# Kernel tuning notes

Measured on AMD Instinct MI355X. Metric: run time of the kernel, lower is better.

The kernel has to match this reference:

```python
import jax, jax.numpy as jnp
import numpy as np

HEADS = 8
DIM_HEAD = 64
SCALE = 10.0
EPS = 1e-12  # F.normalize eps


def setup_inputs() -> dict:
    key = jax.random.key(0)
    k1, k2, k3, k4 = jax.random.split(key, 4)
    dim, hidden = 256, HEADS * DIM_HEAD
    x = jax.random.normal(k1, (8, dim, 32, 32), dtype=jnp.float32)
    w_qkv = jax.random.normal(k2, (3 * hidden, dim), dtype=jnp.float32) * (1.0 / np.sqrt(dim))
    w_out = jax.random.normal(k3, (dim, hidden), dtype=jnp.float32) * (1.0 / np.sqrt(hidden))
    b_out = jax.random.normal(k4, (dim,), dtype=jnp.float32) * 0.01
    return {"x": x, "w_qkv": w_qkv, "w_out": w_out, "b_out": b_out}


def _l2norm_last(t):
    # matches F.normalize(t, dim=-1): t / max(||t||_2, eps)
    n = jnp.sqrt(jnp.sum(t * t, axis=-1, keepdims=True))
    return t / jnp.maximum(n, EPS)


def reference(x, w_qkv, w_out, b_out):
    b, c, hh, ww = x.shape
    n = hh * ww
    # 1x1 conv == channel matmul
    qkv = jnp.einsum('bcxy,oc->boxy', x, w_qkv)  # (b, 3*hidden, h, w)
    q, k, v = jnp.split(qkv, 3, axis=1)
    # 'b (h c) x y -> b h c (x y)'
    to_heads = lambda t: t.reshape(b, HEADS, DIM_HEAD, n)
    q, k, v = to_heads(q), to_heads(k), to_heads(v)
    # NOTE: l2norm over the LAST axis = spatial token axis n (faithful to source)
    q = _l2norm_last(q)
    k = _l2norm_last(k)
    sim = jnp.einsum('bhdi,bhdj->bhij', q, k) * SCALE  # (b, h, n, n)
    attn = jax.nn.softmax(sim, axis=-1)
    out = jnp.einsum('bhij,bhdj->bhid', attn, v)  # (b, h, n, d)
    # 'b h (x y) d -> b (h d) x y'
    out = out.transpose(0, 1, 3, 2).reshape(b, HEADS * DIM_HEAD, hh, ww)
    return jnp.einsum('bcxy,oc->boxy', out, w_out) + b_out[None, :, None, None]
```

## Files before the change

kernel.cpp:

```cpp
#include <hip/hip_runtime.h>
#include <math.h>

#define NHEADS 8
#define DHEAD  64
#define HIDDEN 512
#define CIN    256
#define NTOK   1024
#define QK_SCALE 10.0f
#define LOG2E 1.44269504088896f

typedef __bf16 bf16x8 __attribute__((ext_vector_type(8)));
typedef float  f32x4  __attribute__((ext_vector_type(4)));
typedef unsigned short u16x8 __attribute__((ext_vector_type(8)));

__device__ inline unsigned short f2bf(float f) {
    unsigned u = __builtin_bit_cast(unsigned, f);
    u = (u + 0x7FFFu + ((u >> 16) & 1u)) >> 16;
    return (unsigned short)u;
}

__device__ inline bf16x8 cvt8(const float* p) {
    float4 a = *(const float4*)p;
    float4 b = *(const float4*)(p + 4);
    u16x8 t;
    t[0] = f2bf(a.x); t[1] = f2bf(a.y); t[2] = f2bf(a.z); t[3] = f2bf(a.w);
    t[4] = f2bf(b.x); t[5] = f2bf(b.y); t[6] = f2bf(b.z); t[7] = f2bf(b.w);
    return __builtin_bit_cast(bf16x8, t);
}

__global__ __launch_bounds__(256)
void cvt_x_kernel(const float* __restrict__ x, unsigned short* __restrict__ xt) {
    const int b  = blockIdx.z;
    const int c0 = blockIdx.y * 64;
    const int n0 = blockIdx.x * 64;
    const float* src = x + ((size_t)b * CIN + c0) * NTOK + n0;
    unsigned short* dst = xt + ((size_t)b * NTOK + n0) * CIN + c0;

    __shared__ float T[64][65];
    const int t = threadIdx.x;
    {
        const int nq = t & 15, cg = t >> 4;
        #pragma unroll
        for (int rr = 0; rr < 4; ++rr) {
            const int c = cg + rr * 16;
            float4 v = *(const float4*)(src + (size_t)c * NTOK + nq * 4);
            T[c][nq * 4 + 0] = v.x;
            T[c][nq * 4 + 1] = v.y;
            T[c][nq * 4 + 2] = v.z;
            T[c][nq * 4 + 3] = v.w;
        }
    }
    __syncthreads();
    {
        const int n = t >> 2, cq = t & 3;
        alignas(16) unsigned short tmp[16];
        #pragma unroll
        for (int e = 0; e < 16; ++e)
            tmp[e] = f2bf(T[cq * 16 + e][n]);
        *(uint4*)(dst + (size_t)n * CIN + cq * 16)     = *(uint4*)&tmp[0];
        *(uint4*)(dst + (size_t)n * CIN + cq * 16 + 8) = *(uint4*)&tmp[8];
    }
}

__global__ __launch_bounds__(256)
void cvt_w_kernel(const float* __restrict__ wq, const float* __restrict__ wo,
                  unsigned short* __restrict__ wqb, unsigned short* __restrict__ wob) {
    const size_t i = ((size_t)blockIdx.x * 256 + threadIdx.x) * 8;
    if (i < (size_t)1536 * 256) {
        *(bf16x8*)(wqb + i) = cvt8(wq + i);
    } else {
        const size_t j = i - (size_t)1536 * 256;
        *(bf16x8*)(wob + j) = cvt8(wo + j);
    }
}

__global__ __launch_bounds__(256)
void gemm1_kernel(const unsigned short* __restrict__ wqb,
                  const unsigned short* __restrict__ xt,
                  float* __restrict__ qt,
                  unsigned short* __restrict__ vb,
                  float* __restrict__ ss) {
    const int b  = blockIdx.z;
    const int bm = blockIdx.y * 128;
    const int bn = blockIdx.x * 128;
    const int wave = threadIdx.x >> 6, lane = threadIdx.x & 63;
    const int lo = lane & 15, hi = lane >> 4;
    const int wm = bm + (wave >> 1) * 64;
    const int wn = bn + (wave & 1) * 64;

    const unsigned short* Ab = wqb + (size_t)(wm + lo) * CIN + hi * 8;
    const unsigned short* Bb = xt + ((size_t)b * NTOK + wn + lo) * CIN + hi * 8;

    f32x4 acc[4][4];
    #pragma unroll
    for (int mi = 0; mi < 4; ++mi)
        #pragma unroll
        for (int ni = 0; ni < 4; ++ni) acc[mi][ni] = (f32x4){0.f, 0.f, 0.f, 0.f};

    for (int k0 = 0; k0 < CIN; k0 += 32) {
        bf16x8 a[4], bf[4];
        #pragma unroll
        for (int mi = 0; mi < 4; ++mi) a[mi]  = *(const bf16x8*)(Ab + (size_t)mi * 16 * CIN + k0);
        #pragma unroll
        for (int ni = 0; ni < 4; ++ni) bf[ni] = *(const bf16x8*)(Bb + (size_t)ni * 16 * CIN + k0);
        #pragma unroll
        for (int mi = 0; mi < 4; ++mi)
            #pragma unroll
            for (int ni = 0; ni < 4; ++ni)
                acc[mi][ni] = __builtin_amdgcn_mfma_f32_16x16x32_bf16(a[mi], bf[ni], acc[mi][ni], 0, 0, 0);
    }

    __shared__ unsigned short VL[4][32][72];

    if (bm < 1024) {
        const int isK = (wm >= 512) ? 1 : 0;
        const int ch0 = wm & 511;
        const int head = ch0 >> 6;
        float* dst = qt + (((size_t)isK * 64 + b * 8 + head) * NTOK) * DHEAD;
        #pragma unroll
        for (int mi = 0; mi < 4; ++mi) {
            const int d = mi * 16 + hi * 4;
            #pragma unroll
            for (int ni = 0; ni < 4; ++ni) {
                const int n = wn + ni * 16 + lo;
                *(f32x4*)(dst + (size_t)n * DHEAD + d) = acc[mi][ni];
            }
        }
        float p[4][4];
        #pragma unroll
        for (int mi = 0; mi < 4; ++mi)
            #pragma unroll
            for (int r = 0; r < 4; ++r) {
                float s = 0.f;
                #pragma unroll
                for (int ni = 0; ni < 4; ++ni) s += acc[mi][ni][r] * acc[mi][ni][r];
                p[mi][r] = s;
            }
        #pragma unroll
        for (int off = 1; off < 16; off <<= 1)
            #pragma unroll
            for (int mi = 0; mi < 4; ++mi)
                #pragma unroll
                for (int r = 0; r < 4; ++r)
                    p[mi][r] += __shfl_xor(p[mi][r], off, 64);
        if (lo == 0) {
            #pragma unroll
            for (int mi = 0; mi < 4; ++mi)
                #pragma unroll
                for (int r = 0; r < 4; ++r)
                    atomicAdd(&ss[(size_t)b * 1024 + isK * 512 + ch0 + mi * 16 + hi * 4 + r], p[mi][r]);
        }
    } else {
        const int ch0 = wm - 1024;
        #pragma unroll
        for (int half = 0; half < 2; ++half) {
            #pragma unroll
            for (int mm = 0; mm < 2; ++mm) {
                const int mi = half * 2 + mm;
                #pragma unroll
                for (int ni = 0; ni < 4; ++ni)
                    #pragma unroll
                    for (int r = 0; r < 4; ++r)
                        VL[wave][mm * 16 + hi * 4 + r][ni * 16 + lo] = f2bf(acc[mi][ni][r]);
            }
            #pragma unroll
            for (int i = 0; i < 4; ++i) {
                const int flat = i * 64 + lane;
                const int row = flat >> 3, c = flat & 7;
                uint4 v = *(uint4*)&VL[wave][row][c * 8];
                const int ch = ch0 + half * 32 + row;
                *(uint4*)(vb + ((size_t)b * HIDDEN + ch) * NTOK + wn + c * 8) = v;
            }
        }
    }
}

__global__ __launch_bounds__(256)
void invn_kernel(const float* __restrict__ ss, float* __restrict__ invn) {
    const int i = blockIdx.x * 256 + threadIdx.x;
    invn[i] = 1.0f / fmaxf(sqrtf(ss[i]), 1e-12f);
}

__global__ __launch_bounds__(256)
void scale_cvt_kernel(const float* __restrict__ qt, const float* __restrict__ invn,
                      unsigned short* __restrict__ qs, unsigned short* __restrict__ ks) {
    const size_t idx = ((size_t)blockIdx.x * 256 + threadIdx.x) * 8;
    const size_t half = (size_t)64 * NTOK * DHEAD;
    const int isK = idx >= half;
    const size_t rem = idx - (size_t)isK * half;
    const int bh = (int)(rem >> 16);
    const int d0 = (int)(rem & 63);
    const int b  = bh >> 3;
    const int ch = isK * 512 + (bh & 7) * 64 + d0;
    const float scl = isK ? 1.0f : QK_SCALE;

    const float* ip = qt + idx;
    float4 v0 = *(const float4*)ip;
    float4 v1 = *(const float4*)(ip + 4);
    float4 s0 = *(const float4*)(invn + (size_t)b * 1024 + ch);
    float4 s1 = *(const float4*)(invn + (size_t)b * 1024 + ch + 4);
    u16x8 t;
    t[0] = f2bf(v0.x * s0.x * scl); t[1] = f2bf(v0.y * s0.y * scl);
    t[2] = f2bf(v0.z * s0.z * scl); t[3] = f2bf(v0.w * s0.w * scl);
    t[4] = f2bf(v1.x * s1.x * scl); t[5] = f2bf(v1.y * s1.y * scl);
    t[6] = f2bf(v1.z * s1.z * scl); t[7] = f2bf(v1.w * s1.w * scl);
    *(u16x8*)((isK ? ks : qs) + rem) = t;
}

__global__ __launch_bounds__(256)
void attn_mfma_kernel(const unsigned short* __restrict__ qs,
                      const unsigned short* __restrict__ ks,
                      const unsigned short* __restrict__ vb,
                      unsigned short* __restrict__ attn_t) {
    const int hw = blockIdx.x;
    const int virt = (hw & 7) * 64 + (hw >> 3);
    const int bh = virt >> 3;
    const int it = virt & 7;
    const int b = bh >> 3, h = bh & 7;

    const int lane = threadIdx.x & 63;
    const int wave = threadIdx.x >> 6;
    const int lo = lane & 15;
    const int hi = lane >> 4;
    const int iw = it * 128 + wave * 32;

    const unsigned short* qbh = qs + (size_t)bh * NTOK * DHEAD;
    const unsigned short* kbh = ks + (size_t)bh * NTOK * DHEAD;
    const unsigned short* vbh = vb + ((size_t)b * HIDDEN + h * DHEAD) * NTOK;

    __shared__ unsigned short Plds[4][4096];
    __shared__ float Tlds[4][16][69];
    char* pbase = (char*)&Plds[wave][0];

    bf16x8 aQ[2][2];
    #pragma unroll
    for (int f = 0; f < 2; ++f) {
        const unsigned short* qp = qbh + (size_t)(iw + f * 16 + lo) * DHEAD + hi * 8;
        aQ[f][0] = *(const bf16x8*)qp;
        aQ[f][1] = *(const bf16x8*)(qp + 32);
    }

    float m_r[2][4], l_r[2][4];
    #pragma unroll
    for (int f = 0; f < 2; ++f)
        #pragma unroll
        for (int r = 0; r < 4; ++r) { m_r[f][r] = -INFINITY; l_r[f][r] = 0.0f; }
    f32x4 acc[2][4];
    #pragma unroll
    for (int f = 0; f < 2; ++f)
        #pragma unroll
        for (int ds = 0; ds < 4; ++ds) acc[f][ds] = (f32x4){0.f, 0.f, 0.f, 0.f};

    for (int jt = 0; jt < 8; ++jt) {
        const int j0 = jt * 128;

        f32x4 s[2][8];
        #pragma unroll
        for (int js = 0; js < 8; ++js) {
            const unsigned short* kp = kbh + (size_t)(j0 + js * 16 + lo) * DHEAD + hi * 8;
            const bf16x8 bK0 = *(const bf16x8*)kp;
            const bf16x8 bK1 = *(const bf16x8*)(kp + 32);
            __builtin_amdgcn_s_setprio(1);
            #pragma unroll
            for (int f = 0; f < 2; ++f) {
                f32x4 c = (f32x4){0.f, 0.f, 0.f, 0.f};
                c = __builtin_amdgcn_mfma_f32_16x16x32_bf16(aQ[f][0], bK0, c, 0, 0, 0);
                c = __builtin_amdgcn_mfma_f32_16x16x32_bf16(aQ[f][1], bK1, c, 0, 0, 0);
                s[f][js] = c;
            }
            __builtin_amdgcn_s_setprio(0);
        }

        bf16x8 bV[4][4];
        #pragma unroll
        for (int ds = 0; ds < 4; ++ds)
            #pragma unroll
            for (int jj = 0; jj < 4; ++jj)
                bV[ds][jj] = *(const bf16x8*)(vbh + (size_t)(ds * 16 + lo) * NTOK + j0 + jj * 32 + hi * 8);

        #pragma unroll
        for (int f = 0; f < 2; ++f) {
            float mt[4];
            #pragma unroll
            for (int r = 0; r < 4; ++r)
                mt[r] = fmaxf(fmaxf(fmaxf(s[f][0][r], s[f][1][r]), fmaxf(s[f][2][r], s[f][3][r])),
                              fmaxf(fmaxf(s[f][4][r], s[f][5][r]), fmaxf(s[f][6][r], s[f][7][r])));
            #pragma unroll
            for (int off = 1; off < 16; off <<= 1)
                #pragma unroll
                for (int r = 0; r < 4; ++r)
                    mt[r] = fmaxf(mt[r], __shfl_xor(mt[r], off, 64));

            float corr[4];
            #pragma unroll
            for (int r = 0; r < 4; ++r) {
                const float mn = fmaxf(m_r[f][r], mt[r]);
                corr[r] = __builtin_amdgcn_exp2f((m_r[f][r] - mn) * LOG2E);
                m_r[f][r] = mn;
            }
            float rs[4] = {0.f, 0.f, 0.f, 0.f};
            #pragma unroll
            for (int js = 0; js < 8; ++js)
                #pragma unroll
                for (int r = 0; r < 4; ++r) {
                    const float pp = __builtin_amdgcn_exp2f((s[f][js][r] - m_r[f][r]) * LOG2E);
                    s[f][js][r] = pp;
                    rs[r] += pp;
                }
            #pragma unroll
            for (int off = 1; off < 16; off <<= 1)
                #pragma unroll
                for (int r = 0; r < 4; ++r)
                    rs[r] += __shfl_xor(rs[r], off, 64);
            #pragma unroll
            for (int r = 0; r < 4; ++r) l_r[f][r] = l_r[f][r] * corr[r] + rs[r];
            #pragma unroll
            for (int ds = 0; ds < 4; ++ds)
                #pragma unroll
                for (int r = 0; r < 4; ++r)
                    acc[f][ds][r] *= corr[r];

            #pragma unroll
            for (int js = 0; js < 8; ++js)
                #pragma unroll
                for (int r = 0; r < 4; ++r) {
                    const int row = f * 16 + hi * 4 + r;
                    const int byte = (row * 256 + (js * 16 + lo) * 2) ^ ((row & 7) << 4);
                    *(unsigned short*)(pbase + byte) = f2bf(s[f][js][r]);
                }
        }

        bf16x8 aP[2][4];
        #pragma unroll
        for (int f = 0; f < 2; ++f) {
            const int row = f * 16 + lo;
            const int swz = (lo & 7) << 4;
            #pragma unroll
            for (int jj = 0; jj < 4; ++jj)
                aP[f][jj] = *(const bf16x8*)(pbase + ((row * 256 + jj * 64 + hi * 16) ^ swz));
        }
        __builtin_amdgcn_s_setprio(1);
        #pragma unroll
        for (int ds = 0; ds < 4; ++ds)
            #pragma unroll
            for (int f = 0; f < 2; ++f)
                #pragma unroll
                for (int jj = 0; jj < 4; ++jj)
                    acc[f][ds] = __builtin_amdgcn_mfma_f32_16x16x32_bf16(aP[f][jj], bV[ds][jj], acc[f][ds], 0, 0, 0);
        __builtin_amdgcn_s_setprio(0);
    }

    #pragma unroll
    for (int f = 0; f < 2; ++f) {
        float invl[4];
        #pragma unroll
        for (int r = 0; r < 4; ++r) invl[r] = 1.0f / l_r[f][r];
        #pragma unroll
        for (int ds = 0; ds < 4; ++ds)
            #pragma unroll
            for (int r = 0; r < 4; ++r)
                Tlds[wave][hi * 4 + r][ds * 16 + lo] = acc[f][ds][r] * invl[r];
        {
            const int i = lane >> 2, ck = lane & 3;
            alignas(16) unsigned short tmp[16];
            #pragma unroll
            for (int e = 0; e < 16; ++e)
                tmp[e] = f2bf(Tlds[wave][i][ck * 16 + e]);
            unsigned short* dst = attn_t + ((size_t)b * NTOK + iw + f * 16 + i) * HIDDEN + h * DHEAD + ck * 16;
            *(uint4*)dst       = *(uint4*)&tmp[0];
            *(uint4*)(dst + 8) = *(uint4*)&tmp[8];
        }
    }
}

__global__ __launch_bounds__(128)
void gemm2_kernel(const unsigned short* __restrict__ wob,
                  const unsigned short* __restrict__ attn_t,
                  const float* __restrict__ b_out,
                  float* __restrict__ out) {
    const int b  = blockIdx.z;
    const int bm = blockIdx.y * 64;
    const int bn = blockIdx.x * 128;
    const int wave = threadIdx.x >> 6, lane = threadIdx.x & 63;
    const int lo = lane & 15, hi = lane >> 4;
    const int wn = bn + wave * 64;

    const unsigned short* Ab = wob + (size_t)(bm + lo) * HIDDEN + hi * 8;
    const unsigned short* Bb = attn_t + ((size_t)b * NTOK + wn + lo) * HIDDEN + hi * 8;

    f32x4 acc[4][4];
    #pragma unroll
    for (int mi = 0; mi < 4; ++mi)
        #pragma unroll
        for (int ni = 0; ni < 4; ++ni) acc[mi][ni] = (f32x4){0.f, 0.f, 0.f, 0.f};

    for (int k0 = 0; k0 < HIDDEN; k0 += 32) {
        bf16x8 a[4], bf[4];
        #pragma unroll
        for (int mi = 0; mi < 4; ++mi) a[mi]  = *(const bf16x8*)(Ab + (size_t)mi * 16 * HIDDEN + k0);
        #pragma unroll
        for (int ni = 0; ni < 4; ++ni) bf[ni] = *(const bf16x8*)(Bb + (size_t)ni * 16 * HIDDEN + k0);
        #pragma unroll
        for (int mi = 0; mi < 4; ++mi)
            #pragma unroll
            for (int ni = 0; ni < 4; ++ni)
                acc[mi][ni] = __builtin_amdgcn_mfma_f32_16x16x32_bf16(a[mi], bf[ni], acc[mi][ni], 0, 0, 0);
    }

    __shared__ float OL[2][32][69];
    #pragma unroll
    for (int half = 0; half < 2; ++half) {
        #pragma unroll
        for (int mm = 0; mm < 2; ++mm) {
            const int mi = half * 2 + mm;
            #pragma unroll
            for (int ni = 0; ni < 4; ++ni)
                #pragma unroll
                for (int r = 0; r < 4; ++r)
                    OL[wave][mm * 16 + hi * 4 + r][ni * 16 + lo] = acc[mi][ni][r];
        }
        #pragma unroll
        for (int i = 0; i < 8; ++i) {
            const int flat = i * 64 + lane;
            const int row = flat >> 4, c = flat & 15;
            float4 v = *(float4*)&OL[wave][row][c * 4];
            const int m = bm + half * 32 + row;
            const float bb = b_out[m];
            v.x += bb; v.y += bb; v.z += bb; v.w += bb;
            *(float4*)(out + ((size_t)b * CIN + m) * NTOK + wn + c * 4) = v;
        }
    }
}

extern "C" void kernel_launch(void* const* d_in, const int* in_sizes, int n_in,
                              void* d_out, int out_size, void* d_ws, size_t ws_size,
                              hipStream_t stream) {
    const float* x     = (const float*)d_in[0];
    const float* w_qkv = (const float*)d_in[1];
    const float* w_out = (const float*)d_in[2];
    const float* b_out = (const float*)d_in[3];
    float* out = (float*)d_out;

    char* ws = (char*)d_ws;
    unsigned short* xt  = (unsigned short*)(ws);
    unsigned short* wqb = (unsigned short*)(ws + 4194304);
    unsigned short* wob = (unsigned short*)(ws + 4980736);
    float*          ss  = (float*)(ws + 5242880);
    float*          inv = (float*)(ws + 5275648);
    unsigned short* qs  = (unsigned short*)(ws + 5308416);
    unsigned short* ks  = (unsigned short*)(ws + 13697024);
    unsigned short* vb  = (unsigned short*)(ws + 22085632);
    float*          qt  = (float*)(ws + 30474240);
    unsigned short* attn_t = (unsigned short*)(ws + 30474240);

    hipMemsetAsync(ss, 0, 8 * 1024 * sizeof(float), stream);

    cvt_x_kernel<<<dim3(16, 4, 8), 256, 0, stream>>>(x, xt);
    cvt_w_kernel<<<256, 256, 0, stream>>>(w_qkv, w_out, wqb, wob);

    gemm1_kernel<<<dim3(8, 12, 8), 256, 0, stream>>>(wqb, xt, qt, vb, ss);

    invn_kernel<<<32, 256, 0, stream>>>(ss, inv);
    scale_cvt_kernel<<<4096, 256, 0, stream>>>(qt, inv, qs, ks);

    attn_mfma_kernel<<<512, 256, 0, stream>>>(qs, ks, vb, attn_t);

    gemm2_kernel<<<dim3(8, 4, 8), 128, 0, stream>>>(wob, attn_t, b_out, out);
}
```

Baseline: 218.8 us.

## Split attention over key halves and merge partials in a combine kernel

The attention kernel now splits the key dimension into two halves (split-K flash decoding), doubling the grid from 512 to 1024 blocks and shrinking per-iteration tiles to 64 keys. Each half writes unnormalized fp32 partial outputs plus its row max and sum, and a new combine kernel merges them into bf16 attn_t. The separate invn kernel is folded into scale_cvt, saving a launch. The aim is better occupancy and more blocks across CUs, at the cost of extra fp32 partial traffic and an extra kernel launch.

Measured after the change: 227.4 us. 3.9% more time.

```diff
diff --git a/kernel.cpp b/kernel.cpp
--- a/kernel.cpp
+++ b/kernel.cpp
@@ -12,6 +12,7 @@
 typedef __bf16 bf16x8 __attribute__((ext_vector_type(8)));
 typedef float  f32x4  __attribute__((ext_vector_type(4)));
 typedef unsigned short u16x8 __attribute__((ext_vector_type(8)));
+typedef unsigned short u16x4 __attribute__((ext_vector_type(4)));
 
 __device__ inline unsigned short f2bf(float f) {
     unsigned u = __builtin_bit_cast(unsigned, f);
@@ -176,13 +177,7 @@
 }
 
 __global__ __launch_bounds__(256)
-void invn_kernel(const float* __restrict__ ss, float* __restrict__ invn) {
-    const int i = blockIdx.x * 256 + threadIdx.x;
-    invn[i] = 1.0f / fmaxf(sqrtf(ss[i]), 1e-12f);
-}
-
-__global__ __launch_bounds__(256)
-void scale_cvt_kernel(const float* __restrict__ qt, const float* __restrict__ invn,
+void scale_cvt_kernel(const float* __restrict__ qt, const float* __restrict__ ss,
                       unsigned short* __restrict__ qs, unsigned short* __restrict__ ks) {
     const size_t idx = ((size_t)blockIdx.x * 256 + threadIdx.x) * 8;
     const size_t half = (size_t)64 * NTOK * DHEAD;
@@ -197,8 +192,13 @@
     const float* ip = qt + idx;
     float4 v0 = *(const float4*)ip;
     float4 v1 = *(const float4*)(ip + 4);
-    float4 s0 = *(const float4*)(invn + (size_t)b * 1024 + ch);
-    float4 s1 = *(const float4*)(invn + (size_t)b * 1024 + ch + 4);
+    float4 q0 = *(const float4*)(ss + (size_t)b * 1024 + ch);
+    float4 q1 = *(const float4*)(ss + (size_t)b * 1024 + ch + 4);
+    float4 s0, s1;
+    s0.x = 1.0f / fmaxf(sqrtf(q0.x), 1e-12f); s0.y = 1.0f / fmaxf(sqrtf(q0.y), 1e-12f);
+    s0.z = 1.0f / fmaxf(sqrtf(q0.z), 1e-12f); s0.w = 1.0f / fmaxf(sqrtf(q0.w), 1e-12f);
+    s1.x = 1.0f / fmaxf(sqrtf(q1.x), 1e-12f); s1.y = 1.0f / fmaxf(sqrtf(q1.y), 1e-12f);
+    s1.z = 1.0f / fmaxf(sqrtf(q1.z), 1e-12f); s1.w = 1.0f / fmaxf(sqrtf(q1.w), 1e-12f);
     u16x8 t;
     t[0] = f2bf(v0.x * s0.x * scl); t[1] = f2bf(v0.y * s0.y * scl);
     t[2] = f2bf(v0.z * s0.z * scl); t[3] = f2bf(v0.w * s0.w * scl);
@@ -211,11 +211,13 @@
 void attn_mfma_kernel(const unsigned short* __restrict__ qs,
                       const unsigned short* __restrict__ ks,
                       const unsigned short* __restrict__ vb,
-                      unsigned short* __restrict__ attn_t) {
+                      float* __restrict__ po, float* __restrict__ pml) {
     const int hw = blockIdx.x;
-    const int virt = (hw & 7) * 64 + (hw >> 3);
-    const int bh = virt >> 3;
-    const int it = virt & 7;
+    const int virt = (hw & 7) * 128 + (hw >> 3);
+    const int bh = virt >> 4;
+    const int sub = virt & 15;
+    const int it = sub & 7;
+    const int js = sub >> 3;
     const int b = bh >> 3, h = bh & 7;
 
     const int lane = threadIdx.x & 63;
@@ -228,8 +230,8 @@
     const unsigned short* kbh = ks + (size_t)bh * NTOK * DHEAD;
     const unsigned short* vbh = vb + ((size_t)b * HIDDEN + h * DHEAD) * NTOK;
 
-    __shared__ unsigned short Plds[4][4096];
-    __shared__ float Tlds[4][16][69];
+    __shared__ unsigned short Plds[4][2048];
+    __shared__ float Tlds[4][16][68];
     char* pbase = (char*)&Plds[wave][0];
 
     bf16x8 aQ[2][2];
@@ -252,12 +254,20 @@
         for (int ds = 0; ds < 4; ++ds) acc[f][ds] = (f32x4){0.f, 0.f, 0.f, 0.f};
 
     for (int jt = 0; jt < 8; ++jt) {
-        const int j0 = jt * 128;
-
-        f32x4 s[2][8];
-        #pragma unroll
-        for (int js = 0; js < 8; ++js) {
-            const unsigned short* kp = kbh + (size_t)(j0 + js * 16 + lo) * DHEAD + hi * 8;
+        const int j0 = js * 512 + jt * 64;
+
+        bf16x8 bV[4][2];
+        #pragma unroll
+        for (int ds = 0; ds < 4; ++ds) {
+            const unsigned short* vp = vbh + (size_t)(ds * 16 + lo) * NTOK + j0 + hi * 8;
+            bV[ds][0] = *(const bf16x8*)vp;
+            bV[ds][1] = *(const bf16x8*)(vp + 32);
+        }
+
+        f32x4 s[2][4];
+        #pragma unroll
+        for (int jj = 0; jj < 4; ++jj) {
+            const unsigned short* kp = kbh + (size_t)(j0 + jj * 16 + lo) * DHEAD + hi * 8;
             const bf16x8 bK0 = *(const bf16x8*)kp;
             const bf16x8 bK1 = *(const bf16x8*)(kp + 32);
             __builtin_amdgcn_s_setprio(1);
@@ -266,25 +276,17 @@
                 f32x4 c = (f32x4){0.f, 0.f, 0.f, 0.f};
                 c = __builtin_amdgcn_mfma_f32_16x16x32_bf16(aQ[f][0], bK0, c, 0, 0, 0);
                 c = __builtin_amdgcn_mfma_f32_16x16x32_bf16(aQ[f][1], bK1, c, 0, 0, 0);
-                s[f][js] = c;
+                s[f][jj] = c;
             }
             __builtin_amdgcn_s_setprio(0);
         }
-
-        bf16x8 bV[4][4];
-        #pragma unroll
-        for (int ds = 0; ds < 4; ++ds)
-            #pragma unroll
-            for (int jj = 0; jj < 4; ++jj)
-                bV[ds][jj] = *(const bf16x8*)(vbh + (size_t)(ds * 16 + lo) * NTOK + j0 + jj * 32 + hi * 8);
 
         #pragma unroll
         for (int f = 0; f < 2; ++f) {
             float mt[4];
             #pragma unroll
             for (int r = 0; r < 4; ++r)
-                mt[r] = fmaxf(fmaxf(fmaxf(s[f][0][r], s[f][1][r]), fmaxf(s[f][2][r], s[f][3][r])),
-                              fmaxf(fmaxf(s[f][4][r], s[f][5][r]), fmaxf(s[f][6][r], s[f][7][r])));
+                mt[r] = fmaxf(fmaxf(s[f][0][r], s[f][1][r]), fmaxf(s[f][2][r], s[f][3][r]));
             #pragma unroll
             for (int off = 1; off < 16; off <<= 1)
                 #pragma unroll
@@ -300,11 +302,11 @@
             }
             float rs[4] = {0.f, 0.f, 0.f, 0.f};
             #pragma unroll
-            for (int js = 0; js < 8; ++js)
+            for (int jj = 0; jj < 4; ++jj)
                 #pragma unroll
                 for (int r = 0; r < 4; ++r) {
-                    const float pp = __builtin_amdgcn_exp2f((s[f][js][r] - m_r[f][r]) * LOG2E);
-                    s[f][js][r] = pp;
+                    const float pp = __builtin_amdgcn_exp2f((s[f][jj][r] - m_r[f][r]) * LOG2E);
+                    s[f][jj][r] = pp;
                     rs[r] += pp;
                 }
             #pragma unroll
@@ -321,56 +323,86 @@
                     acc[f][ds][r] *= corr[r];
 
             #pragma unroll
-            for (int js = 0; js < 8; ++js)
+            for (int jj = 0; jj < 4; ++jj)
                 #pragma unroll
                 for (int r = 0; r < 4; ++r) {
                     const int row = f * 16 + hi * 4 + r;
-                    const int byte = (row * 256 + (js * 16 + lo) * 2) ^ ((row & 7) << 4);
-                    *(unsigned short*)(pbase + byte) = f2bf(s[f][js][r]);
+                    const int byte = (row * 128 + (jj * 16 + lo) * 2) ^ ((row & 7) << 4);
+                    *(unsigned short*)(pbase + byte) = f2bf(s[f][jj][r]);
                 }
         }
 
-        bf16x8 aP[2][4];
+        bf16x8 aP[2][2];
         #pragma unroll
         for (int f = 0; f < 2; ++f) {
             const int row = f * 16 + lo;
             const int swz = (lo & 7) << 4;
-            #pragma unroll
-            for (int jj = 0; jj < 4; ++jj)
-                aP[f][jj] = *(const bf16x8*)(pbase + ((row * 256 + jj * 64 + hi * 16) ^ swz));
+            aP[f][0] = *(const bf16x8*)(pbase + ((row * 128 + hi * 16) ^ swz));
+            aP[f][1] = *(const bf16x8*)(pbase + ((row * 128 + 64 + hi * 16) ^ swz));
         }
         __builtin_amdgcn_s_setprio(1);
         #pragma unroll
         for (int ds = 0; ds < 4; ++ds)
             #pragma unroll
-            for (int f = 0; f < 2; ++f)
-                #pragma unroll
-                for (int jj = 0; jj < 4; ++jj)
-                    acc[f][ds] = __builtin_amdgcn_mfma_f32_16x16x32_bf16(aP[f][jj], bV[ds][jj], acc[f][ds], 0, 0, 0);
+            for (int f = 0; f < 2; ++f) {
+                acc[f][ds] = __builtin_amdgcn_mfma_f32_16x16x32_bf16(aP[f][0], bV[ds][0], acc[f][ds], 0, 0, 0);
+                acc[f][ds] = __builtin_amdgcn_mfma_f32_16x16x32_bf16(aP[f][1], bV[ds][1], acc[f][ds], 0, 0, 0);
+            }
         __builtin_amdgcn_s_setprio(0);
     }
 
+    float* pob = po + ((size_t)(js * 64 + bh) * NTOK + iw) * DHEAD;
     #pragma unroll
     for (int f = 0; f < 2; ++f) {
-        float invl[4];
-        #pragma unroll
-        for (int r = 0; r < 4; ++r) invl[r] = 1.0f / l_r[f][r];
         #pragma unroll
         for (int ds = 0; ds < 4; ++ds)
             #pragma unroll
             for (int r = 0; r < 4; ++r)
-                Tlds[wave][hi * 4 + r][ds * 16 + lo] = acc[f][ds][r] * invl[r];
-        {
-            const int i = lane >> 2, ck = lane & 3;
-            alignas(16) unsigned short tmp[16];
-            #pragma unroll
-            for (int e = 0; e < 16; ++e)
-                tmp[e] = f2bf(Tlds[wave][i][ck * 16 + e]);
-            unsigned short* dst = attn_t + ((size_t)b * NTOK + iw + f * 16 + i) * HIDDEN + h * DHEAD + ck * 16;
-            *(uint4*)dst       = *(uint4*)&tmp[0];
-            *(uint4*)(dst + 8) = *(uint4*)&tmp[8];
-        }
-    }
+                Tlds[wave][hi * 4 + r][ds * 16 + lo] = acc[f][ds][r];
+        #pragma unroll
+        for (int pass = 0; pass < 4; ++pass) {
+            const int flat = pass * 64 + lane;
+            const int row = flat >> 4, dq = flat & 15;
+            float4 v = *(float4*)&Tlds[wave][row][dq * 4];
+            *(float4*)(pob + (size_t)(f * 16 + row) * DHEAD + dq * 4) = v;
+        }
+        if (lo == 0) {
+            #pragma unroll
+            for (int r = 0; r < 4; ++r) {
+                const int row = iw + f * 16 + hi * 4 + r;
+                float2 ml = make_float2(m_r[f][r], l_r[f][r]);
+                *(float2*)(pml + ((size_t)(js * 64 + bh) * NTOK + row) * 2) = ml;
+            }
+        }
+    }
+}
+
+__global__ __launch_bounds__(256)
+void combine_kernel(const float* __restrict__ po, const float* __restrict__ pml,
+                    unsigned short* __restrict__ attn_t) {
+    const size_t fl = ((size_t)blockIdx.x * 256 + threadIdx.x) * 4;
+    const int bh  = (int)(fl >> 16);
+    const int rem = (int)(fl & 65535);
+    const int row = rem >> 6;
+    const int d   = rem & 63;
+    const int b = bh >> 3, h = bh & 7;
+    const size_t SS = (size_t)64 * NTOK * DHEAD;
+
+    const float2 ml1 = *(const float2*)(pml + ((size_t)bh * NTOK + row) * 2);
+    const float2 ml2 = *(const float2*)(pml + ((size_t)(64 + bh) * NTOK + row) * 2);
+    const float M  = fmaxf(ml1.x, ml2.x);
+    const float w1 = __builtin_amdgcn_exp2f((ml1.x - M) * LOG2E);
+    const float w2 = __builtin_amdgcn_exp2f((ml2.x - M) * LOG2E);
+    const float inv = 1.0f / (ml1.y * w1 + ml2.y * w2);
+
+    const float4 o1 = *(const float4*)(po + fl);
+    const float4 o2 = *(const float4*)(po + SS + fl);
+    u16x4 r;
+    r[0] = f2bf((o1.x * w1 + o2.x * w2) * inv);
+    r[1] = f2bf((o1.y * w1 + o2.y * w2) * inv);
+    r[2] = f2bf((o1.z * w1 + o2.z * w2) * inv);
+    r[3] = f2bf((o1.w * w1 + o2.w * w2) * inv);
+    *(u16x4*)(attn_t + ((size_t)b * NTOK + row) * HIDDEN + h * DHEAD + d) = r;
 }
 
 __global__ __launch_bounds__(128)
@@ -446,12 +478,13 @@
     unsigned short* wqb = (unsigned short*)(ws + 4194304);
     unsigned short* wob = (unsigned short*)(ws + 4980736);
     float*          ss  = (float*)(ws + 5242880);
-    float*          inv = (float*)(ws + 5275648);
     unsigned short* qs  = (unsigned short*)(ws + 5308416);
     unsigned short* ks  = (unsigned short*)(ws + 13697024);
     unsigned short* vb  = (unsigned short*)(ws + 22085632);
     float*          qt  = (float*)(ws + 30474240);
-    unsigned short* attn_t = (unsigned short*)(ws + 30474240);
+    float*          po  = (float*)(ws + 30474240);
+    unsigned short* attn_t = (unsigned short*)(ws + 5308416);
+    float*          pml = (float*)(ws + 64028672);
 
     hipMemsetAsync(ss, 0, 8 * 1024 * sizeof(float), stream);
 
@@ -460,10 +493,11 @@
 
     gemm1_kernel<<<dim3(8, 12, 8), 256, 0, stream>>>(wqb, xt, qt, vb, ss);
 
-    invn_kernel<<<32, 256, 0, stream>>>(ss, inv);
-    scale_cvt_kernel<<<4096, 256, 0, stream>>>(qt, inv, qs, ks);
-
-    attn_mfma_kernel<<<512, 256, 0, stream>>>(qs, ks, vb, attn_t);
+    scale_cvt_kernel<<<4096, 256, 0, stream>>>(qt, ss, qs, ks);
+
+    attn_mfma_kernel<<<1024, 256, 0, stream>>>(qs, ks, vb, po, pml);
+
+    combine_kernel<<<4096, 256, 0, stream>>>(po, pml, attn_t);
 
     gemm2_kernel<<<dim3(8, 4, 8), 128, 0, stream>>>(wob, attn_t, b_out, out);
 }
```
